# Kernel tuning notes

Hardware: AMD Instinct MI355X
Metric: run time of the kernel (lower is better)

The kernel has to match this reference:

```python
import jax, jax.numpy as jnp
import numpy as np

T, B, D, H, O = 512, 256, 85, 512, 33
SIGMA = 0.05


def setup_inputs() -> dict:
    key = jax.random.key(0)
    ks = jax.random.split(key, 16)
    sD = 1.0 / np.sqrt(D)
    sH = 1.0 / np.sqrt(H)
    # orthogonal init for W_hh (randortho), scaled by rec_scale_factor=1.0
    A = np.asarray(jax.random.normal(ks[10], (H, H), jnp.float32))
    Q, _ = np.linalg.qr(A)
    return {
        "x": jax.random.normal(ks[0], (T, B, D), jnp.float32),
        "r_noise": jax.random.uniform(ks[1], (T, B, D), jnp.float32) * SIGMA,
        "z_noise": jax.random.uniform(ks[2], (T, B, D), jnp.float32) * SIGMA,
        "h_noise": jax.random.uniform(ks[3], (T, B, D), jnp.float32) * SIGMA,
        "W_xr": jax.random.uniform(ks[4], (H, D), jnp.float32, -sD, sD),
        "W_xz": jax.random.uniform(ks[5], (H, D), jnp.float32, -sD, sD),
        "W_xh": jax.random.uniform(ks[6], (H, D), jnp.float32, -sD, sD),
        "W_hr": jax.random.uniform(ks[7], (H, H), jnp.float32, -sH, sH),
        "b_hr": jax.random.uniform(ks[8], (H,), jnp.float32, -sH, sH),
        "W_hz": jax.random.uniform(ks[9], (H, H), jnp.float32, -sH, sH),
        "b_hz": jax.random.uniform(ks[11], (H,), jnp.float32, -sH, sH),
        "W_hh": jnp.asarray(Q, jnp.float32),
        "b_hh": jax.random.uniform(ks[12], (H,), jnp.float32, -sH, sH),
        "W_ro": jax.random.uniform(ks[13], (O, H), jnp.float32, -sH, sH),
        "b_ro": jax.random.uniform(ks[14], (O,), jnp.float32, -sH, sH),
    }


def reference(x, r_noise, z_noise, h_noise,
              W_xr, W_xz, W_xh,
              W_hr, b_hr, W_hz, b_hz, W_hh, b_hh,
              W_ro, b_ro):
    # Precompute all input-to-hidden projections in three big GEMMs [T,B,H]
    xr = jnp.einsum('tbd,hd->tbh', x + r_noise, W_xr)
    xz = jnp.einsum('tbd,hd->tbh', x + z_noise, W_xz)
    xh = jnp.einsum('tbd,hd->tbh', x + h_noise, W_xh)

    def step(h, inputs):
        xr_t, xz_t, xh_t = inputs
        R = jax.nn.sigmoid(xr_t + h @ W_hr.T + b_hr)
        Z = jax.nn.sigmoid(xz_t + h @ W_hz.T + b_hz)
        H_hat = jnp.tanh(xh_t + (R * h) @ W_hh.T + b_hh)
        h_new = Z * h + (1.0 - Z) * H_hat
        return h_new, h_new

    h0 = jnp.zeros((x.shape[1], W_hh.shape[0]), x.dtype)
    _, hs = jax.lax.scan(step, h0, (xr, xz, xh))  # hs: [T,B,H]
    out = jnp.einsum('tbh,oh->tbo', hs, W_ro) + b_ro  # [T,B,O]
    return out
```

## Files before the change

### kernel.cpp

```cpp
#include <hip/hip_runtime.h>
#include <stdint.h>

#define TSTEPS 512
#define NB     256
#define DIN    85
#define DPAD   96
#define HID    512
#define ODIM   33
#define OPAD   48
#define TBROWS (TSTEPS*NB)
#define NBLK   256
#define SROWS  16

typedef unsigned int u32;
typedef unsigned short u16;
typedef unsigned long long u64;
typedef __bf16 bf16x8 __attribute__((ext_vector_type(8)));
typedef float  f32x4  __attribute__((ext_vector_type(4)));

__device__ __forceinline__ u16 f2bf(float f) {
  u32 u = __float_as_uint(f);
  return (u16)((u + 0x7FFFu + ((u >> 16) & 1u)) >> 16);
}
__device__ __forceinline__ float bf2f(u16 h) {
  return __uint_as_float(((u32)h) << 16);
}
__device__ __forceinline__ bf16x8 bc8(uint4 v) { return __builtin_bit_cast(bf16x8, v); }
__device__ __forceinline__ f32x4 mfma_bf16(bf16x8 a, bf16x8 b, f32x4 c) {
  return __builtin_amdgcn_mfma_f32_16x16x32_bf16(a, b, c, 0, 0, 0);
}
__device__ __forceinline__ float fsigmoid(float x) { return 1.0f / (1.0f + __expf(-x)); }
__device__ __forceinline__ float ftanh(float x)    { return 2.0f / (1.0f + __expf(-2.0f*x)) - 1.0f; }

__device__ __forceinline__ void st_u32_llc(u32* p, u32 v) {
  __hip_atomic_store(p, v, __ATOMIC_RELAXED, __HIP_MEMORY_SCOPE_AGENT);
}
__device__ __forceinline__ u32 ld_u32_llc(const u32* p) {
  return __hip_atomic_load(p, __ATOMIC_RELAXED, __HIP_MEMORY_SCOPE_AGENT);
}
__device__ __forceinline__ u64 ld_u64_llc(const u64* p) {
  return __hip_atomic_load(p, __ATOMIC_RELAXED, __HIP_MEMORY_SCOPE_AGENT);
}
__device__ __forceinline__ void st_f32_llc(float* p, float v) {
  __hip_atomic_store(p, v, __ATOMIC_RELAXED, __HIP_MEMORY_SCOPE_AGENT);
}
__device__ __forceinline__ float ld_f32_llc(const float* p) {
  return __hip_atomic_load(p, __ATOMIC_RELAXED, __HIP_MEMORY_SCOPE_AGENT);
}

__global__ void __launch_bounds__(256) prep_kernel(
    const float* __restrict__ Whr, const float* __restrict__ Whz, const float* __restrict__ Whh,
    const float* __restrict__ Wxr, const float* __restrict__ Wxz, const float* __restrict__ Wxh,
    const float* __restrict__ Wro,
    u16* __restrict__ w_hb, u16* __restrict__ wx_hi, u16* __restrict__ wx_lo,
    u16* __restrict__ w_rob)
{
  int tid = blockIdx.x * blockDim.x + threadIdx.x;
  int np  = gridDim.x * blockDim.x;
  for (int i = tid; i < 3 * HID * HID; i += np) {
    int m = i / (HID * HID), r = i % (HID * HID);
    const float* src = (m == 0) ? Whr : ((m == 1) ? Whz : Whh);
    w_hb[i] = f2bf(src[r]);
  }
  for (int i = tid; i < 3 * HID * DPAD; i += np) {
    int m = i / (HID * DPAD), r = i % (HID * DPAD);
    int row = r / DPAD, k = r % DPAD;
    const float* src = (m == 0) ? Wxr : ((m == 1) ? Wxz : Wxh);
    u16 hi = 0, lo = 0;
    if (k < DIN) {
      float v = src[row * DIN + k];
      hi = f2bf(v);
      lo = f2bf(v - bf2f(hi));
    }
    wx_hi[i] = hi; wx_lo[i] = lo;
  }
  for (int i = tid; i < OPAD * HID; i += np) {
    int row = i / HID, k = i % HID;
    w_rob[i] = (row < ODIM) ? f2bf(Wro[row * HID + k]) : (u16)0;
  }
}

#define LROW 520

__global__ void __launch_bounds__(256, 1) recur_kernel(
    const float* __restrict__ x,  const float* __restrict__ nr,
    const float* __restrict__ nz, const float* __restrict__ nh,
    const float* __restrict__ bhr, const float* __restrict__ bhz, const float* __restrict__ bhh,
    const u16* __restrict__ wx_hi, const u16* __restrict__ wx_lo, const u16* __restrict__ w_hb,
    u32* __restrict__ h_pk, u32* __restrict__ g_pk,
    float* __restrict__ z_buf, u32* __restrict__ flags,
    u16* __restrict__ hs_out,
    const float* __restrict__ Wro, const float* __restrict__ bro, float* __restrict__ out,
    int do_c)
{
  __shared__ __attribute__((aligned(16))) u16 sBig[2 * SROWS * LROW];
  __shared__ __attribute__((aligned(16))) u16 sXh[SROWS][104];
  __shared__ __attribute__((aligned(16))) u16 sXl[SROWS][104];
  __shared__ __attribute__((aligned(16))) float sC[2][64][4];

  u16 (*sHh)[LROW] = (u16(*)[LROW])sBig;
  u16 (*sHl)[LROW] = (u16(*)[LROW])(sBig + SROWS * LROW);
  u16 (*sGh)[LROW] = sHh;
  u16 (*sGl)[LROW] = sHl;
  float* sC2 = (float*)sBig;

  const int bid  = blockIdx.x;
  const int tid  = threadIdx.x;
  const int lane = tid & 63;
  const int wave = tid >> 6;
  const int strip = bid & 15;
  const int part  = bid >> 4;

  u32* gflag = flags + strip * 16;

  const int isZ = part >= 8;
  const int ncA = (part & 7) * 64;
  const u16*  WA   = w_hb  + (size_t)(isZ ? 1 : 0) * HID * HID;
  const u16*  WXAh = wx_hi + (size_t)(isZ ? 1 : 0) * HID * DPAD;
  const u16*  WXAl = wx_lo + (size_t)(isZ ? 1 : 0) * HID * DPAD;
  const float* nA  = isZ ? nz : nr;
  const int rowl  = lane & 15;
  const int colA  = ncA + wave * 16 + rowl;
  const float biasA = (isZ ? bhz : bhr)[colA];

  const int ncB  = part * 32;
  const u16*  WH   = w_hb  + (size_t)2 * HID * HID;
  const u16*  WXBh = wx_hi + (size_t)2 * HID * DPAD;
  const u16*  WXBl = wx_lo + (size_t)2 * HID * DPAD;
  const int ntB = wave & 1;
  const int khB = wave >> 1;
  const int colB = ncB + ntB * 16 + rowl;
  const float biasB = bhh[colB];

  float h_old[4] = {0.f, 0.f, 0.f, 0.f};

  for (int c = tid; c < SROWS * (104 - DIN); c += 256) {
    int row = c / (104 - DIN), k = DIN + c % (104 - DIN);
    sXh[row][k] = 0; sXl[row][k] = 0;
  }
  {
    const size_t xoff = (size_t)(strip * SROWS) * DIN;
    for (int c = tid; c < SROWS * DIN; c += 256) {
      int row = c / DIN, k = c - row * DIN;
      float v = x[xoff + c] + nA[xoff + c];
      u16 hi = f2bf(v);
      sXh[row][k] = hi;
      sXl[row][k] = f2bf(v - bf2f(hi));
    }
  }

  for (int t = 1; t <= TSTEPS; ++t) {
    if (do_c && t >= 2) {
      const int row = strip * SROWS + (part);
      const int o = tid >> 3, q = tid & 7;
      const int base = row * HID + q * 64;
      float a = 0.f;
      #pragma unroll 8
      for (int k2 = 0; k2 < 64; ++k2) {
        u32 v = ld_u32_llc(&h_pk[base + k2]);
        a += (bf2f((u16)(v >> 16)) + bf2f((u16)(v & 0xFFFFu))) * Wro[(size_t)o * HID + q * 64 + k2];
      }
      __syncthreads();
      sC2[o * 8 + q] = a;
      if (tid < 8) {
        float a2 = 0.f;
        const int base2 = row * HID + tid * 64;
        #pragma unroll 8
        for (int k2 = 0; k2 < 64; ++k2) {
          u32 v = ld_u32_llc(&h_pk[base2 + k2]);
          a2 += (bf2f((u16)(v >> 16)) + bf2f((u16)(v & 0xFFFFu))) * Wro[(size_t)32 * HID + tid * 64 + k2];
        }
        sC2[32 * 8 + tid] = a2;
      }
      __syncthreads();
      if (tid < ODIM) {
        float s = bro[tid];
        #pragma unroll
        for (int q2 = 0; q2 < 8; ++q2) s += sC2[tid * 8 + q2];
        out[(size_t)((t - 2) * NB + row) * ODIM + tid] = s;
      }
      __syncthreads();
    }

    {
      const u64* hsrc = (const u64*)h_pk;
      u64 hreg[SROWS];
      #pragma unroll
      for (int i = 0; i < SROWS; ++i)
        hreg[i] = ld_u64_llc(&hsrc[(size_t)(strip * SROWS + i) * 256 + tid]);
      #pragma unroll
      for (int i = 0; i < SROWS; ++i) {
        u32 v0 = (u32)hreg[i], v1 = (u32)(hreg[i] >> 32);
        *(u32*)&sHh[i][tid * 2] = (v0 >> 16) | (v1 & 0xFFFF0000u);
        *(u32*)&sHl[i][tid * 2] = (v0 & 0xFFFFu) | (v1 << 16);
      }
    }
    __syncthreads();

    f32x4 accA = {0.f, 0.f, 0.f, 0.f};
    #pragma unroll
    for (int ks = 0; ks < 3; ++ks) {
      int kk = ks * 32 + 8 * (lane >> 4);
      bf16x8 wh = bc8(*(const uint4*)&WXAh[(size_t)colA * DPAD + kk]);
      bf16x8 wl = bc8(*(const uint4*)&WXAl[(size_t)colA * DPAD + kk]);
      bf16x8 xh = bc8(*(const uint4*)&sXh[rowl][kk]);
      bf16x8 xl = bc8(*(const uint4*)&sXl[rowl][kk]);
      accA = mfma_bf16(xh, wh, accA);
      accA = mfma_bf16(xl, wh, accA);
      accA = mfma_bf16(xh, wl, accA);
    }
    #pragma unroll
    for (int kk16 = 0; kk16 < 16; ++kk16) {
      int k = kk16 * 32 + 8 * (lane >> 4);
      bf16x8 bw = bc8(*(const uint4*)&WA[(size_t)colA * HID + k]);
      bf16x8 ah = bc8(*(const uint4*)&sHh[rowl][k]);
      bf16x8 al = bc8(*(const uint4*)&sHl[rowl][k]);
      accA = mfma_bf16(ah, bw, accA);
      accA = mfma_bf16(al, bw, accA);
    }

    #pragma unroll
    for (int r = 0; r < 4; ++r) {
      int rowm = (lane >> 4) * 4 + r;
      int grow = strip * SROWS + rowm;
      float val = fsigmoid(accA[r] + biasA);
      size_t idx = (size_t)grow * HID + colA;
      if (!isZ) {
        float hcur = bf2f(sHh[rowm][colA]) + bf2f(sHl[rowm][colA]);
        float g = val * hcur;
        u16 gh = f2bf(g);
        u16 gl = f2bf(g - bf2f(gh));
        st_u32_llc(&g_pk[idx], ((u32)gh << 16) | (u32)gl);
      } else {
        st_f32_llc(&z_buf[idx], val);
      }
    }

    __syncthreads();
    if (tid == 0) st_u32_llc(&gflag[part], (u32)(2 * t - 1));

    {
      const size_t xoff = (size_t)((t - 1) * NB + strip * SROWS) * DIN;
      for (int c = tid; c < SROWS * DIN; c += 256) {
        int row = c / DIN, k = c - row * DIN;
        float v = x[xoff + c] + nh[xoff + c];
        u16 hi = f2bf(v);
        sXh[row][k] = hi;
        sXl[row][k] = f2bf(v - bf2f(hi));
      }
    }
    if (wave == 0) {
      const u32 target = (u32)(2 * t - 1);
      for (;;) {
        u32 a = (lane < 16) ? ld_u32_llc(&gflag[lane]) : target;
        if (__all(a >= target)) break;
      }
    }
    __syncthreads();

    float zv[4];
    if (khB == 0) {
      #pragma unroll
      for (int r = 0; r < 4; ++r) {
        int brow = strip * SROWS + (lane >> 4) * 4 + r;
        zv[r] = ld_f32_llc(&z_buf[(size_t)brow * HID + colB]);
      }
    }
    {
      const u64* gsrc = (const u64*)g_pk;
      u64 greg[SROWS];
      #pragma unroll
      for (int i = 0; i < SROWS; ++i)
        greg[i] = ld_u64_llc(&gsrc[(size_t)(strip * SROWS + i) * 256 + tid]);
      #pragma unroll
      for (int i = 0; i < SROWS; ++i) {
        u32 v0 = (u32)greg[i], v1 = (u32)(greg[i] >> 32);
        *(u32*)&sGh[i][tid * 2] = (v0 >> 16) | (v1 & 0xFFFF0000u);
        *(u32*)&sGl[i][tid * 2] = (v0 & 0xFFFFu) | (v1 << 16);
      }
    }
    __syncthreads();

    f32x4 accB = {0.f, 0.f, 0.f, 0.f};
    if (khB == 0) {
      #pragma unroll
      for (int ks = 0; ks < 3; ++ks) {
        int kk = ks * 32 + 8 * (lane >> 4);
        bf16x8 wh = bc8(*(const uint4*)&WXBh[(size_t)colB * DPAD + kk]);
        bf16x8 wl = bc8(*(const uint4*)&WXBl[(size_t)colB * DPAD + kk]);
        bf16x8 xh = bc8(*(const uint4*)&sXh[rowl][kk]);
        bf16x8 xl = bc8(*(const uint4*)&sXl[rowl][kk]);
        accB = mfma_bf16(xh, wh, accB);
        accB = mfma_bf16(xl, wh, accB);
        accB = mfma_bf16(xh, wl, accB);
      }
    }
    #pragma unroll
    for (int f = 0; f < 8; ++f) {
      int k = khB * 256 + f * 32 + 8 * (lane >> 4);
      bf16x8 bw = bc8(*(const uint4*)&WH[(size_t)colB * HID + k]);
      bf16x8 gh = bc8(*(const uint4*)&sGh[rowl][k]);
      bf16x8 gl = bc8(*(const uint4*)&sGl[rowl][k]);
      accB = mfma_bf16(gh, bw, accB);
      accB = mfma_bf16(gl, bw, accB);
    }
    if (khB == 1) *(f32x4*)&sC[ntB][lane][0] = accB;
    __syncthreads();

    if (khB == 0) {
      f32x4 oth = *(const f32x4*)&sC[ntB][lane][0];
      accB[0] += oth[0]; accB[1] += oth[1]; accB[2] += oth[2]; accB[3] += oth[3];
      #pragma unroll
      for (int r = 0; r < 4; ++r) {
        int brow = strip * SROWS + (lane >> 4) * 4 + r;
        float hh = ftanh(accB[r] + biasB);
        float hn = zv[r] * h_old[r] + (1.0f - zv[r]) * hh;
        h_old[r] = hn;
        u16 hi = f2bf(hn);
        u16 lo = f2bf(hn - bf2f(hi));
        st_u32_llc(&h_pk[(size_t)brow * HID + colB], ((u32)hi << 16) | (u32)lo);
        if (hs_out)
          hs_out[(size_t)((t - 1) * NB + brow) * HID + colB] = hi;
      }
    }

    __syncthreads();
    if (tid == 0) st_u32_llc(&gflag[part], (u32)(2 * t));

    if (t < TSTEPS) {
      const size_t xoff = (size_t)(t * NB + strip * SROWS) * DIN;
      for (int c = tid; c < SROWS * DIN; c += 256) {
        int row = c / DIN, k = c - row * DIN;
        float v = x[xoff + c] + nA[xoff + c];
        u16 hi = f2bf(v);
        sXh[row][k] = hi;
        sXl[row][k] = f2bf(v - bf2f(hi));
      }
    }
    if (wave == 0) {
      const u32 target = (u32)(2 * t);
      for (;;) {
        u32 a = (lane < 16) ? ld_u32_llc(&gflag[lane]) : target;
        if (__all(a >= target)) break;
      }
    }
    __syncthreads();
  }

  if (do_c) {
    const int row = strip * SROWS + part;
    const int o = tid >> 3, q = tid & 7;
    const int base = row * HID + q * 64;
    float a = 0.f;
    #pragma unroll 8
    for (int k2 = 0; k2 < 64; ++k2) {
      u32 v = ld_u32_llc(&h_pk[base + k2]);
      a += (bf2f((u16)(v >> 16)) + bf2f((u16)(v & 0xFFFFu))) * Wro[(size_t)o * HID + q * 64 + k2];
    }
    __syncthreads();
    sC2[o * 8 + q] = a;
    if (tid < 8) {
      float a2 = 0.f;
      const int base2 = row * HID + tid * 64;
      #pragma unroll 8
      for (int k2 = 0; k2 < 64; ++k2) {
        u32 v = ld_u32_llc(&h_pk[base2 + k2]);
        a2 += (bf2f((u16)(v >> 16)) + bf2f((u16)(v & 0xFFFFu))) * Wro[(size_t)32 * HID + tid * 64 + k2];
      }
      sC2[32 * 8 + tid] = a2;
    }
    __syncthreads();
    if (tid < ODIM) {
      float s = bro[tid];
      #pragma unroll
      for (int q2 = 0; q2 < 8; ++q2) s += sC2[tid * 8 + q2];
      out[(size_t)((TSTEPS - 1) * NB + row) * ODIM + tid] = s;
    }
  }
}

__global__ void __launch_bounds__(256) out_kernel(
    const u16* __restrict__ hs_out,
    const u16* __restrict__ w_rob, const float* __restrict__ b_ro,
    float* __restrict__ out)
{
  __shared__ __attribute__((aligned(16))) u16 sOh[128][72];

  const int m0   = blockIdx.x * 128;
  const int tid  = threadIdx.x;
  const int lane = tid & 63, wave = tid >> 6;

  f32x4 acc[2][3];
  for (int a = 0; a < 2; ++a) for (int b = 0; b < 3; ++b) acc[a][b] = {0.f, 0.f, 0.f, 0.f};

  for (int kc = 0; kc < 8; ++kc) {
    __syncthreads();
    #pragma unroll
    for (int i = 0; i < 4; ++i) {
      int c = tid + 256 * i; int row = c >> 3, seg = c & 7;
      *(uint4*)&sOh[row][seg * 8] =
        *(const uint4*)&hs_out[(size_t)(m0 + row) * HID + kc * 64 + seg * 8];
    }
    __syncthreads();
    #pragma unroll
    for (int ks = 0; ks < 2; ++ks) {
      int klocal = ks * 32 + 8 * (lane >> 4);
      int kglob  = kc * 64 + klocal;
      bf16x8 ah[2];
      #pragma unroll
      for (int mf = 0; mf < 2; ++mf) {
        int rowl = wave * 32 + mf * 16 + (lane & 15);
        ah[mf] = bc8(*(const uint4*)&sOh[rowl][klocal]);
      }
      #pragma unroll
      for (int nf = 0; nf < 3; ++nf) {
        int wrow = nf * 16 + (lane & 15);
        bf16x8 bw = bc8(*(const uint4*)&w_rob[(size_t)wrow * HID + kglob]);
        #pragma unroll
        for (int mf = 0; mf < 2; ++mf)
          acc[mf][nf] = mfma_bf16(ah[mf], bw, acc[mf][nf]);
      }
    }
  }
  for (int nf = 0; nf < 3; ++nf) {
    int o = nf * 16 + (lane & 15);
    if (o < ODIM) {
      float bb = b_ro[o];
      for (int mf = 0; mf < 2; ++mf)
        for (int r = 0; r < 4; ++r) {
          int R = m0 + wave * 32 + mf * 16 + (lane >> 4) * 4 + r;
          out[(size_t)R * ODIM + o] = acc[mf][nf][r] + bb;
        }
    }
  }
}

extern "C" void kernel_launch(void* const* d_in, const int* in_sizes, int n_in,
                              void* d_out, int out_size, void* d_ws, size_t ws_size,
                              hipStream_t stream)
{
  const float* x   = (const float*)d_in[0];
  const float* nr  = (const float*)d_in[1];
  const float* nz  = (const float*)d_in[2];
  const float* nh  = (const float*)d_in[3];
  const float* Wxr = (const float*)d_in[4];
  const float* Wxz = (const float*)d_in[5];
  const float* Wxh = (const float*)d_in[6];
  const float* Whr = (const float*)d_in[7];
  const float* bhr = (const float*)d_in[8];
  const float* Whz = (const float*)d_in[9];
  const float* bhz = (const float*)d_in[10];
  const float* Whh = (const float*)d_in[11];
  const float* bhh = (const float*)d_in[12];
  const float* Wro = (const float*)d_in[13];
  const float* bro = (const float*)d_in[14];
  float* out = (float*)d_out;

  char* ws = (char*)d_ws;
  size_t off = 0;
  auto alloc = [&](size_t bytes) -> char* {
    char* p = ws + off;
    off += (bytes + 255) & ~(size_t)255;
    return p;
  };
  u32*  h_pk  = (u32*) alloc((size_t)NB * HID * 4);
  u32*  g_pk  = (u32*) alloc((size_t)NB * HID * 4);
  float* z_buf= (float*)alloc((size_t)NB * HID * 4);
  u16*  w_hb  = (u16*) alloc((size_t)3 * HID * HID * 2);
  u16*  wx_hi = (u16*) alloc((size_t)3 * HID * DPAD * 2);
  u16*  wx_lo = (u16*) alloc((size_t)3 * HID * DPAD * 2);
  u16*  w_rob = (u16*) alloc((size_t)OPAD * HID * 2);
  u32*  flags = (u32*) alloc((size_t)16 * 16 * 4);
  size_t small_need = off;
  if (ws_size < small_need) return;

  u16* hs_out = (u16*)(ws + off);
  size_t big_need = off + (size_t)TBROWS * HID * 2 + 256;
  bool big = (ws_size >= big_need);
  if (!big) hs_out = nullptr;

  hipMemsetAsync(flags, 0, (size_t)16 * 16 * 4, stream);
  hipMemsetAsync(h_pk,  0, (size_t)NB * HID * 4, stream);

  prep_kernel<<<512, 256, 0, stream>>>(Whr, Whz, Whh, Wxr, Wxz, Wxh, Wro,
                                       w_hb, wx_hi, wx_lo, w_rob);

  recur_kernel<<<NBLK, 256, 0, stream>>>(
      x, nr, nz, nh, bhr, bhz, bhh, wx_hi, wx_lo, w_hb,
      h_pk, g_pk, z_buf, flags, hs_out, Wro, bro, out, big ? 0 : 1);

  if (big)
    out_kernel<<<TBROWS / 128, 256, 0, stream>>>(hs_out, w_rob, bro, out);
}
```

Baseline: 5.271 ms.

## Replace per-phase flag barriers with tagged double-buffered data polling

The two group-wide flag barriers per timestep are replaced by a generation tag packed into the low bit of each stored value (h, g, z), with h, g and z double-buffered by timestep parity. Consumers poll the data itself until the tags match, and a lagged progress counter per block only guards against buffer reuse two steps ahead. This removes most barrier round-trips and flag polling from the serial critical path. In exchange it gives up one mantissa bit of the low bf16 part and of z, adds spin loops over many loads, and doubles the workspace.

```diff
diff --git a/kernel.cpp b/kernel.cpp
--- a/kernel.cpp
+++ b/kernel.cpp
@@ -41,12 +41,8 @@
 __device__ __forceinline__ u64 ld_u64_llc(const u64* p) {
   return __hip_atomic_load(p, __ATOMIC_RELAXED, __HIP_MEMORY_SCOPE_AGENT);
 }
-__device__ __forceinline__ void st_f32_llc(float* p, float v) {
-  __hip_atomic_store(p, v, __ATOMIC_RELAXED, __HIP_MEMORY_SCOPE_AGENT);
-}
-__device__ __forceinline__ float ld_f32_llc(const float* p) {
-  return __hip_atomic_load(p, __ATOMIC_RELAXED, __HIP_MEMORY_SCOPE_AGENT);
-}
+
+__device__ __forceinline__ u32 gen_tag(int t) { return 1u ^ (((u32)(t - 1) >> 1) & 1u); }
 
 __global__ void __launch_bounds__(256) prep_kernel(
     const float* __restrict__ Whr, const float* __restrict__ Whz, const float* __restrict__ Whh,
@@ -87,15 +83,17 @@
     const float* __restrict__ nz, const float* __restrict__ nh,
     const float* __restrict__ bhr, const float* __restrict__ bhz, const float* __restrict__ bhh,
     const u16* __restrict__ wx_hi, const u16* __restrict__ wx_lo, const u16* __restrict__ w_hb,
-    u32* __restrict__ h_pk, u32* __restrict__ g_pk,
-    float* __restrict__ z_buf, u32* __restrict__ flags,
+    u32* __restrict__ h_pk, u32* __restrict__ g_pk, u32* __restrict__ z_pk,
+    u32* __restrict__ flags,
     u16* __restrict__ hs_out,
     const float* __restrict__ Wro, const float* __restrict__ bro, float* __restrict__ out,
     int do_c)
 {
   __shared__ __attribute__((aligned(16))) u16 sBig[2 * SROWS * LROW];
-  __shared__ __attribute__((aligned(16))) u16 sXh[SROWS][104];
-  __shared__ __attribute__((aligned(16))) u16 sXl[SROWS][104];
+  __shared__ __attribute__((aligned(16))) u16 sXAh[SROWS][104];
+  __shared__ __attribute__((aligned(16))) u16 sXAl[SROWS][104];
+  __shared__ __attribute__((aligned(16))) u16 sXBh[SROWS][104];
+  __shared__ __attribute__((aligned(16))) u16 sXBl[SROWS][104];
   __shared__ __attribute__((aligned(16))) float sC[2][64][4];
 
   u16 (*sHh)[LROW] = (u16(*)[LROW])sBig;
@@ -111,7 +109,7 @@
   const int strip = bid & 15;
   const int part  = bid >> 4;
 
-  u32* gflag = flags + strip * 16;
+  u32* gprog = flags + strip * 16;
 
   const int isZ = part >= 8;
   const int ncA = (part & 7) * 64;
@@ -136,7 +134,7 @@
 
   for (int c = tid; c < SROWS * (104 - DIN); c += 256) {
     int row = c / (104 - DIN), k = DIN + c % (104 - DIN);
-    sXh[row][k] = 0; sXl[row][k] = 0;
+    sXAh[row][k] = 0; sXAl[row][k] = 0; sXBh[row][k] = 0; sXBl[row][k] = 0;
   }
   {
     const size_t xoff = (size_t)(strip * SROWS) * DIN;
@@ -144,31 +142,54 @@
       int row = c / DIN, k = c - row * DIN;
       float v = x[xoff + c] + nA[xoff + c];
       u16 hi = f2bf(v);
-      sXh[row][k] = hi;
-      sXl[row][k] = f2bf(v - bf2f(hi));
+      sXAh[row][k] = hi;
+      sXAl[row][k] = f2bf(v - bf2f(hi));
     }
   }
 
   for (int t = 1; t <= TSTEPS; ++t) {
+    const u32 tg = gen_tag(t);
+    const u32 hexp = (t == 1) ? 0u : gen_tag(t - 1);
+
     if (do_c && t >= 2) {
-      const int row = strip * SROWS + (part);
+      const int row = strip * SROWS + part;
       const int o = tid >> 3, q = tid & 7;
-      const int base = row * HID + q * 64;
+      const u32* hp = h_pk + (size_t)((t - 1) & 1) * NB * HID + (size_t)row * HID + q * 64;
       float a = 0.f;
-      #pragma unroll 8
-      for (int k2 = 0; k2 < 64; ++k2) {
-        u32 v = ld_u32_llc(&h_pk[base + k2]);
-        a += (bf2f((u16)(v >> 16)) + bf2f((u16)(v & 0xFFFFu))) * Wro[(size_t)o * HID + q * 64 + k2];
+      #pragma unroll
+      for (int c8 = 0; c8 < 8; ++c8) {
+        u32 vv[8];
+        #pragma unroll
+        for (int j = 0; j < 8; ++j) vv[j] = ld_u32_llc(&hp[c8 * 8 + j]);
+        for (;;) {
+          bool ok = true;
+          #pragma unroll
+          for (int j = 0; j < 8; ++j) ok = ok && ((vv[j] & 1u) == hexp);
+          if (__all(ok)) break;
+          #pragma unroll
+          for (int j = 0; j < 8; ++j) vv[j] = ld_u32_llc(&hp[c8 * 8 + j]);
+        }
+        #pragma unroll
+        for (int j = 0; j < 8; ++j) {
+          float hv = bf2f((u16)(vv[j] >> 16)) + bf2f((u16)(vv[j] & 0xFFFEu));
+          a += hv * Wro[(size_t)o * HID + q * 64 + c8 * 8 + j];
+        }
       }
       __syncthreads();
       sC2[o * 8 + q] = a;
       if (tid < 8) {
+        const u32* hp2 = h_pk + (size_t)((t - 1) & 1) * NB * HID + (size_t)row * HID + tid * 64;
         float a2 = 0.f;
-        const int base2 = row * HID + tid * 64;
-        #pragma unroll 8
-        for (int k2 = 0; k2 < 64; ++k2) {
-          u32 v = ld_u32_llc(&h_pk[base2 + k2]);
-          a2 += (bf2f((u16)(v >> 16)) + bf2f((u16)(v & 0xFFFFu))) * Wro[(size_t)32 * HID + tid * 64 + k2];
+        #pragma unroll
+        for (int c8 = 0; c8 < 8; ++c8) {
+          u32 vv[8];
+          #pragma unroll
+          for (int j = 0; j < 8; ++j) vv[j] = ld_u32_llc(&hp2[c8 * 8 + j]);
+          #pragma unroll
+          for (int j = 0; j < 8; ++j) {
+            float hv = bf2f((u16)(vv[j] >> 16)) + bf2f((u16)(vv[j] & 0xFFFEu));
+            a2 += hv * Wro[(size_t)32 * HID + tid * 64 + c8 * 8 + j];
+          }
         }
         sC2[32 * 8 + tid] = a2;
       }
@@ -182,18 +203,35 @@
       __syncthreads();
     }
 
-    {
-      const u64* hsrc = (const u64*)h_pk;
-      u64 hreg[SROWS];
+    const u64* hsrc = (const u64*)(h_pk + (size_t)((t - 1) & 1) * NB * HID);
+    u64 hreg[SROWS];
+    #pragma unroll
+    for (int i = 0; i < SROWS; ++i)
+      hreg[i] = ld_u64_llc(&hsrc[(size_t)(strip * SROWS + i) * 256 + tid]);
+
+    if (wave == 0 && t > 2) {
+      const u32 target = (u32)(t - 2);
+      for (;;) {
+        u32 a = (lane < 16) ? ld_u32_llc(&gprog[lane]) : target;
+        if (__all(a >= target)) break;
+      }
+    }
+
+    for (;;) {
+      bool ok = true;
+      #pragma unroll
+      for (int i = 0; i < SROWS; ++i)
+        ok = ok && (((u32)hreg[i] & 1u) == hexp) && (((u32)(hreg[i] >> 32) & 1u) == hexp);
+      if (__all(ok)) break;
       #pragma unroll
       for (int i = 0; i < SROWS; ++i)
         hreg[i] = ld_u64_llc(&hsrc[(size_t)(strip * SROWS + i) * 256 + tid]);
-      #pragma unroll
-      for (int i = 0; i < SROWS; ++i) {
-        u32 v0 = (u32)hreg[i], v1 = (u32)(hreg[i] >> 32);
-        *(u32*)&sHh[i][tid * 2] = (v0 >> 16) | (v1 & 0xFFFF0000u);
-        *(u32*)&sHl[i][tid * 2] = (v0 & 0xFFFFu) | (v1 << 16);
-      }
+    }
+    #pragma unroll
+    for (int i = 0; i < SROWS; ++i) {
+      u32 v0 = (u32)hreg[i], v1 = (u32)(hreg[i] >> 32);
+      *(u32*)&sHh[i][tid * 2] = (v0 >> 16) | (v1 & 0xFFFF0000u);
+      *(u32*)&sHl[i][tid * 2] = (v0 & 0xFFFEu) | ((v1 & 0xFFFEu) << 16);
     }
     __syncthreads();
 
@@ -203,8 +241,8 @@
       int kk = ks * 32 + 8 * (lane >> 4);
       bf16x8 wh = bc8(*(const uint4*)&WXAh[(size_t)colA * DPAD + kk]);
       bf16x8 wl = bc8(*(const uint4*)&WXAl[(size_t)colA * DPAD + kk]);
-      bf16x8 xh = bc8(*(const uint4*)&sXh[rowl][kk]);
-      bf16x8 xl = bc8(*(const uint4*)&sXl[rowl][kk]);
+      bf16x8 xh = bc8(*(const uint4*)&sXAh[rowl][kk]);
+      bf16x8 xl = bc8(*(const uint4*)&sXAl[rowl][kk]);
       accA = mfma_bf16(xh, wh, accA);
       accA = mfma_bf16(xl, wh, accA);
       accA = mfma_bf16(xh, wl, accA);
@@ -219,25 +257,42 @@
       accA = mfma_bf16(al, bw, accA);
     }
 
-    #pragma unroll
-    for (int r = 0; r < 4; ++r) {
-      int rowm = (lane >> 4) * 4 + r;
-      int grow = strip * SROWS + rowm;
-      float val = fsigmoid(accA[r] + biasA);
-      size_t idx = (size_t)grow * HID + colA;
-      if (!isZ) {
-        float hcur = bf2f(sHh[rowm][colA]) + bf2f(sHl[rowm][colA]);
-        float g = val * hcur;
-        u16 gh = f2bf(g);
-        u16 gl = f2bf(g - bf2f(gh));
-        st_u32_llc(&g_pk[idx], ((u32)gh << 16) | (u32)gl);
-      } else {
-        st_f32_llc(&z_buf[idx], val);
-      }
-    }
-
-    __syncthreads();
-    if (tid == 0) st_u32_llc(&gflag[part], (u32)(2 * t - 1));
+    {
+      u32* gdst = g_pk + (size_t)(t & 1) * NB * HID;
+      u32* zdst = z_pk + (size_t)(t & 1) * NB * HID;
+      #pragma unroll
+      for (int r = 0; r < 4; ++r) {
+        int rowm = (lane >> 4) * 4 + r;
+        int grow = strip * SROWS + rowm;
+        float val = fsigmoid(accA[r] + biasA);
+        size_t idx = (size_t)grow * HID + colA;
+        if (!isZ) {
+          float hcur = bf2f(sHh[rowm][colA]) + bf2f(sHl[rowm][colA]);
+          float g = val * hcur;
+          u16 gh = f2bf(g);
+          u16 gl = f2bf(g - bf2f(gh));
+          st_u32_llc(&gdst[idx], ((u32)gh << 16) | ((u32)gl & 0xFFFEu) | tg);
+        } else {
+          st_u32_llc(&zdst[idx], (__float_as_uint(val) & ~1u) | tg);
+        }
+      }
+    }
+
+    const u64* gsrc = (const u64*)(g_pk + (size_t)(t & 1) * NB * HID);
+    u64 greg[SROWS];
+    #pragma unroll
+    for (int i = 0; i < SROWS; ++i)
+      greg[i] = ld_u64_llc(&gsrc[(size_t)(strip * SROWS + i) * 256 + tid]);
+
+    u32 zr[4];
+    if (khB == 0) {
+      const u32* zsrc = z_pk + (size_t)(t & 1) * NB * HID;
+      #pragma unroll
+      for (int r = 0; r < 4; ++r) {
+        int brow = strip * SROWS + (lane >> 4) * 4 + r;
+        zr[r] = ld_u32_llc(&zsrc[(size_t)brow * HID + colB]);
+      }
+    }
 
     {
       const size_t xoff = (size_t)((t - 1) * NB + strip * SROWS) * DIN;
@@ -245,41 +300,52 @@
         int row = c / DIN, k = c - row * DIN;
         float v = x[xoff + c] + nh[xoff + c];
         u16 hi = f2bf(v);
-        sXh[row][k] = hi;
-        sXl[row][k] = f2bf(v - bf2f(hi));
-      }
-    }
-    if (wave == 0) {
-      const u32 target = (u32)(2 * t - 1);
+        sXBh[row][k] = hi;
+        sXBl[row][k] = f2bf(v - bf2f(hi));
+      }
+    }
+
+    if (wave == 0 && t > 1) {
+      const u32 target = (u32)(t - 1);
       for (;;) {
-        u32 a = (lane < 16) ? ld_u32_llc(&gflag[lane]) : target;
+        u32 a = (lane < 16) ? ld_u32_llc(&gprog[lane]) : target;
         if (__all(a >= target)) break;
       }
     }
-    __syncthreads();
-
-    float zv[4];
+
     if (khB == 0) {
-      #pragma unroll
-      for (int r = 0; r < 4; ++r) {
-        int brow = strip * SROWS + (lane >> 4) * 4 + r;
-        zv[r] = ld_f32_llc(&z_buf[(size_t)brow * HID + colB]);
-      }
-    }
-    {
-      const u64* gsrc = (const u64*)g_pk;
-      u64 greg[SROWS];
+      const u32* zsrc = z_pk + (size_t)(t & 1) * NB * HID;
+      for (;;) {
+        bool ok = true;
+        #pragma unroll
+        for (int r = 0; r < 4; ++r) ok = ok && ((zr[r] & 1u) == tg);
+        if (__all(ok)) break;
+        #pragma unroll
+        for (int r = 0; r < 4; ++r) {
+          int brow = strip * SROWS + (lane >> 4) * 4 + r;
+          zr[r] = ld_u32_llc(&zsrc[(size_t)brow * HID + colB]);
+        }
+      }
+    }
+    for (;;) {
+      bool ok = true;
+      #pragma unroll
+      for (int i = 0; i < SROWS; ++i)
+        ok = ok && (((u32)greg[i] & 1u) == tg) && (((u32)(greg[i] >> 32) & 1u) == tg);
+      if (__all(ok)) break;
       #pragma unroll
       for (int i = 0; i < SROWS; ++i)
         greg[i] = ld_u64_llc(&gsrc[(size_t)(strip * SROWS + i) * 256 + tid]);
-      #pragma unroll
-      for (int i = 0; i < SROWS; ++i) {
-        u32 v0 = (u32)greg[i], v1 = (u32)(greg[i] >> 32);
-        *(u32*)&sGh[i][tid * 2] = (v0 >> 16) | (v1 & 0xFFFF0000u);
-        *(u32*)&sGl[i][tid * 2] = (v0 & 0xFFFFu) | (v1 << 16);
-      }
-    }
-    __syncthreads();
+    }
+    #pragma unroll
+    for (int i = 0; i < SROWS; ++i) {
+      u32 v0 = (u32)greg[i], v1 = (u32)(greg[i] >> 32);
+      *(u32*)&sGh[i][tid * 2] = (v0 >> 16) | (v1 & 0xFFFF0000u);
+      *(u32*)&sGl[i][tid * 2] = (v0 & 0xFFFEu) | ((v1 & 0xFFFEu) << 16);
+    }
+    __syncthreads();
+
+    if (tid == 0) st_u32_llc(&gprog[part], (u32)t);
 
     f32x4 accB = {0.f, 0.f, 0.f, 0.f};
     if (khB == 0) {
@@ -288,8 +354,8 @@
         int kk = ks * 32 + 8 * (lane >> 4);
         bf16x8 wh = bc8(*(const uint4*)&WXBh[(size_t)colB * DPAD + kk]);
         bf16x8 wl = bc8(*(const uint4*)&WXBl[(size_t)colB * DPAD + kk]);
-        bf16x8 xh = bc8(*(const uint4*)&sXh[rowl][kk]);
-        bf16x8 xl = bc8(*(const uint4*)&sXl[rowl][kk]);
+        bf16x8 xh = bc8(*(const uint4*)&sXBh[rowl][kk]);
+        bf16x8 xl = bc8(*(const uint4*)&sXBl[rowl][kk]);
         accB = mfma_bf16(xh, wh, accB);
         accB = mfma_bf16(xl, wh, accB);
         accB = mfma_bf16(xh, wl, accB);
@@ -310,22 +376,21 @@
     if (khB == 0) {
       f32x4 oth = *(const f32x4*)&sC[ntB][lane][0];
       accB[0] += oth[0]; accB[1] += oth[1]; accB[2] += oth[2]; accB[3] += oth[3];
+      u32* hdst = h_pk + (size_t)(t & 1) * NB * HID;
       #pragma unroll
       for (int r = 0; r < 4; ++r) {
         int brow = strip * SROWS + (lane >> 4) * 4 + r;
+        float z = __uint_as_float(zr[r] & ~1u);
         float hh = ftanh(accB[r] + biasB);
-        float hn = zv[r] * h_old[r] + (1.0f - zv[r]) * hh;
+        float hn = z * h_old[r] + (1.0f - z) * hh;
         h_old[r] = hn;
         u16 hi = f2bf(hn);
         u16 lo = f2bf(hn - bf2f(hi));
-        st_u32_llc(&h_pk[(size_t)brow * HID + colB], ((u32)hi << 16) | (u32)lo);
+        st_u32_llc(&hdst[(size_t)brow * HID + colB], ((u32)hi << 16) | ((u32)lo & 0xFFFEu) | tg);
         if (hs_out)
           hs_out[(size_t)((t - 1) * NB + brow) * HID + colB] = hi;
       }
     }
-
-    __syncthreads();
-    if (tid == 0) st_u32_llc(&gflag[part], (u32)(2 * t));
 
     if (t < TSTEPS) {
       const size_t xoff = (size_t)(t * NB + strip * SROWS) * DIN;
@@ -333,39 +398,53 @@
         int row = c / DIN, k = c - row * DIN;
         float v = x[xoff + c] + nA[xoff + c];
         u16 hi = f2bf(v);
-        sXh[row][k] = hi;
-        sXl[row][k] = f2bf(v - bf2f(hi));
-      }
-    }
-    if (wave == 0) {
-      const u32 target = (u32)(2 * t);
-      for (;;) {
-        u32 a = (lane < 16) ? ld_u32_llc(&gflag[lane]) : target;
-        if (__all(a >= target)) break;
-      }
-    }
-    __syncthreads();
+        sXAh[row][k] = hi;
+        sXAl[row][k] = f2bf(v - bf2f(hi));
+      }
+    }
   }
 
   if (do_c) {
+    const int t = TSTEPS + 1;
+    const u32 hexp = gen_tag(t - 1);
     const int row = strip * SROWS + part;
     const int o = tid >> 3, q = tid & 7;
-    const int base = row * HID + q * 64;
+    const u32* hp = h_pk + (size_t)((t - 1) & 1) * NB * HID + (size_t)row * HID + q * 64;
     float a = 0.f;
-    #pragma unroll 8
-    for (int k2 = 0; k2 < 64; ++k2) {
-      u32 v = ld_u32_llc(&h_pk[base + k2]);
-      a += (bf2f((u16)(v >> 16)) + bf2f((u16)(v & 0xFFFFu))) * Wro[(size_t)o * HID + q * 64 + k2];
+    #pragma unroll
+    for (int c8 = 0; c8 < 8; ++c8) {
+      u32 vv[8];
+      #pragma unroll
+      for (int j = 0; j < 8; ++j) vv[j] = ld_u32_llc(&hp[c8 * 8 + j]);
+      for (;;) {
+        bool ok = true;
+        #pragma unroll
+        for (int j = 0; j < 8; ++j) ok = ok && ((vv[j] & 1u) == hexp);
+        if (__all(ok)) break;
+        #pragma unroll
+        for (int j = 0; j < 8; ++j) vv[j] = ld_u32_llc(&hp[c8 * 8 + j]);
+      }
+      #pragma unroll
+      for (int j = 0; j < 8; ++j) {
+        float hv = bf2f((u16)(vv[j] >> 16)) + bf2f((u16)(vv[j] & 0xFFFEu));
+        a += hv * Wro[(size_t)o * HID + q * 64 + c8 * 8 + j];
+      }
     }
     __syncthreads();
     sC2[o * 8 + q] = a;
     if (tid < 8) {
+      const u32* hp2 = h_pk + (size_t)((t - 1) & 1) * NB * HID + (size_t)row * HID + tid * 64;
       float a2 = 0.f;
-      const int base2 = row * HID + tid * 64;
-      #pragma unroll 8
-      for (int k2 = 0; k2 < 64; ++k2) {
-        u32 v = ld_u32_llc(&h_pk[base2 + k2]);
-        a2 += (bf2f((u16)(v >> 16)) + bf2f((u16)(v & 0xFFFFu))) * Wro[(size_t)32 * HID + tid * 64 + k2];
+      #pragma unroll
+      for (int c8 = 0; c8 < 8; ++c8) {
+        u32 vv[8];
+        #pragma unroll
+        for (int j = 0; j < 8; ++j) vv[j] = ld_u32_llc(&hp2[c8 * 8 + j]);
+        #pragma unroll
+        for (int j = 0; j < 8; ++j) {
+          float hv = bf2f((u16)(vv[j] >> 16)) + bf2f((u16)(vv[j] & 0xFFFEu));
+          a2 += hv * Wro[(size_t)32 * HID + tid * 64 + c8 * 8 + j];
+        }
       }
       sC2[32 * 8 + tid] = a2;
     }
@@ -463,9 +542,9 @@
     off += (bytes + 255) & ~(size_t)255;
     return p;
   };
-  u32*  h_pk  = (u32*) alloc((size_t)NB * HID * 4);
-  u32*  g_pk  = (u32*) alloc((size_t)NB * HID * 4);
-  float* z_buf= (float*)alloc((size_t)NB * HID * 4);
+  u32*  h_pk  = (u32*) alloc((size_t)2 * NB * HID * 4);
+  u32*  g_pk  = (u32*) alloc((size_t)2 * NB * HID * 4);
+  u32*  z_pk  = (u32*) alloc((size_t)2 * NB * HID * 4);
   u16*  w_hb  = (u16*) alloc((size_t)3 * HID * HID * 2);
   u16*  wx_hi = (u16*) alloc((size_t)3 * HID * DPAD * 2);
   u16*  wx_lo = (u16*) alloc((size_t)3 * HID * DPAD * 2);
@@ -487,7 +566,7 @@
 
   recur_kernel<<<NBLK, 256, 0, stream>>>(
       x, nr, nz, nh, bhr, bhz, bhh, wx_hi, wx_lo, w_hb,
-      h_pk, g_pk, z_buf, flags, hs_out, Wro, bro, out, big ? 0 : 1);
+      h_pk, g_pk, z_pk, flags, hs_out, Wro, bro, out, big ? 0 : 1);
 
   if (big)
     out_kernel<<<TBROWS / 128, 256, 0, stream>>>(hs_out, w_rob, bro, out);
```

After: 6.353 ms. 20.5% more time.
